# Kernel optimization log

Measured on AMD Instinct MI355X. Metric: run time of the kernel, lower is better.

The kernel has to match this reference:

```python
import jax, jax.numpy as jnp
import numpy as np

MARGIN_SCALE = 0.2
SPATIAL_ALPHA = 0.6
CHANNEL_ALPHA = 0.5
LANG_ALPHA = 0.4
EPS = 1e-06


def _xywh_to_xyxy(boxes):
    xc, yc, w, h = jnp.split(boxes, 4, axis=-1)
    return jnp.concatenate([xc - w / 2.0, yc - h / 2.0, xc + w / 2.0, yc + h / 2.0], axis=-1)


def _clamp_boxes(boxes):
    x1, y1, x2, y2 = [jnp.clip(b[..., 0], 0.0, 1.0) for b in jnp.split(boxes, 4, axis=-1)]
    x_low, x_high = jnp.minimum(x1, x2), jnp.maximum(x1, x2)
    y_low, y_high = jnp.minimum(y1, y2), jnp.maximum(y1, y2)
    w = jnp.maximum(x_high - x_low, EPS)
    h = jnp.maximum(y_high - y_low, EPS)
    cx = (x_high + x_low) * 0.5
    cy = (y_high + y_low) * 0.5
    return jnp.stack([
        jnp.clip(cx - w * 0.5, 0.0, 1.0),
        jnp.clip(cy - h * 0.5, 0.0, 1.0),
        jnp.clip(cx + w * 0.5, 0.0, 1.0),
        jnp.clip(cy + h * 0.5, 0.0, 1.0),
    ], axis=-1)


def _box_to_mask(boxes_xyxy, H, W, margin, dtype):
    # fully vectorized replacement of the per-sample Python loop
    ys = jnp.linspace(0.0, 1.0, H)  # [H]
    xs = jnp.linspace(0.0, 1.0, W)  # [W]
    x1, y1, x2, y2 = [boxes_xyxy[:, i] for i in range(4)]
    mx1 = jnp.clip(x1 - margin, 0.0, 1.0)[:, None, None]
    my1 = jnp.clip(y1 - margin, 0.0, 1.0)[:, None, None]
    mx2 = jnp.clip(x2 + margin, 0.0, 1.0)[:, None, None]
    my2 = jnp.clip(y2 + margin, 0.0, 1.0)[:, None, None]
    xg = xs[None, None, :]  # [1,1,W]
    yg = ys[None, :, None]  # [1,H,1]
    mask = (xg >= mx1) & (xg <= mx2) & (yg >= my1) & (yg <= my2)  # [B,H,W]
    return mask.astype(dtype)[:, None, :, :]  # [B,1,H,W]


def _conv2d(x, w, b, pad):
    out = jax.lax.conv_general_dilated(
        x, w, window_strides=(1, 1), padding=((pad, pad), (pad, pad)),
        dimension_numbers=('NCHW', 'OIHW', 'NCHW'))
    return out + b[None, :, None, None]


def setup_inputs() -> dict:
    key = jax.random.key(0)
    ks = jax.random.split(key, 9)
    B, C, H, W = 32, 256, 64, 64
    s = lambda fan_in: 1.0 / np.sqrt(fan_in)
    return {
        'feat': jax.random.normal(ks[0], (B, C, H, W), jnp.float32),
        'lang_vec': jax.random.normal(ks[1], (B, 256), jnp.float32),
        'pointer_xywh': jax.random.uniform(ks[2], (B, 4), jnp.float32),
        'conv1_w': jax.random.normal(ks[3], (16, 1, 3, 3), jnp.float32) * s(9),
        'conv1_b': jnp.zeros((16,), jnp.float32),
        'conv2_w': jax.random.normal(ks[4], (1, 16, 1, 1), jnp.float32) * s(16),
        'conv2_b': jnp.zeros((1,), jnp.float32),
        'cg_w1': jax.random.normal(ks[5], (256, 512), jnp.float32) * s(512),
        'cg_b1': jnp.zeros((256,), jnp.float32),
        'cg_w2': jax.random.normal(ks[6], (256, 256), jnp.float32) * s(256),
        'cg_b2': jnp.zeros((256,), jnp.float32),
        'lf_w1': jax.random.normal(ks[7], (256, 512), jnp.float32) * s(512),
        'lf_b1': jnp.zeros((256,), jnp.float32),
        'lf_w2': jax.random.normal(ks[8], (256, 256), jnp.float32) * s(256),
        'lf_b2': jnp.zeros((256,), jnp.float32),
    }


def reference(feat, lang_vec, pointer_xywh, conv1_w, conv1_b, conv2_w, conv2_b,
              cg_w1, cg_b1, cg_w2, cg_b2, lf_w1, lf_b1, lf_w2, lf_b2):
    B, C, H, W = feat.shape
    boxes_xyxy = _clamp_boxes(_xywh_to_xyxy(pointer_xywh))
    w = jnp.maximum(boxes_xyxy[:, 2] - boxes_xyxy[:, 0], 1e-4)
    h = jnp.maximum(boxes_xyxy[:, 3] - boxes_xyxy[:, 1], 1e-4)
    diag = jnp.sqrt(w * w + h * h)
    margin = jnp.clip(diag * MARGIN_SCALE, 0.02, 0.2)
    mask = _box_to_mask(boxes_xyxy, H, W, margin, feat.dtype)  # [B,1,H,W]

    # spatial gate: conv3x3 -> relu -> conv1x1 -> sigmoid
    hidden = jax.nn.relu(_conv2d(mask, conv1_w, conv1_b, pad=1))
    refined_mask = jax.nn.sigmoid(_conv2d(hidden, conv2_w, conv2_b, pad=0))  # [B,1,H,W]

    mask_area = jnp.maximum(refined_mask.sum(axis=(2, 3)), 1.0)  # [B,1]
    pointer_feat = (feat * refined_mask).sum(axis=(2, 3)) / mask_area  # [B,C]

    fusion = jnp.concatenate([pointer_feat, lang_vec], axis=1)  # [B, C+256]
    ch_gate = jax.nn.sigmoid(jax.nn.relu(fusion @ cg_w1.T + cg_b1) @ cg_w2.T + cg_b2)
    ch_gate = ch_gate.reshape(B, C, 1, 1)
    lang_delta = jnp.tanh(jax.nn.relu(fusion @ lf_w1.T + lf_b1) @ lf_w2.T + lf_b2)

    guided_feat = feat * (1.0 + SPATIAL_ALPHA * refined_mask) * (1.0 + CHANNEL_ALPHA * ch_gate)
    guided_lang = lang_vec + LANG_ALPHA * lang_delta
    return (guided_feat, guided_lang, boxes_xyxy, refined_mask, pointer_feat)
```

## Files before the change

### kernel.cpp

```cpp
#include <hip/hip_runtime.h>
#include <math.h>

#define B_  32
#define C_  256
#define H_  64
#define W_  64
#define HW  (H_*W_)
#define HW4 (HW/4)
#define RPB 4

typedef float f32x4 __attribute__((ext_vector_type(4)));

__device__ __forceinline__ float clamp01(float v) {
    return fminf(fmaxf(v, 0.0f), 1.0f);
}

__global__ __launch_bounds__(256) void kern_pf(
    const float* __restrict__ feat, const float* __restrict__ xywh,
    const float* __restrict__ conv1_w, const float* __restrict__ conv1_b,
    const float* __restrict__ conv2_w, const float* __restrict__ conv2_b,
    float* __restrict__ out_boxes, float* __restrict__ out_rm,
    float* __restrict__ out_pf)
{
    const int blk = blockIdx.x;
    const int b = blk >> 6;
    const int g = blk & 63;
    const int c0 = g * RPB;
    const int t = threadIdx.x;

    __shared__ float sw1[16 * 9];
    __shared__ float sb1[16];
    __shared__ float sw2[16];
    __shared__ float tbl[64];
    __shared__ int   xpat[64];
    __shared__ int   ypat[64];
    __shared__ f32x4 rm4_lds[HW4];
    __shared__ float sreda[4];
    __shared__ f32x4 sredv[4];

    float* rm_lds = (float*)rm4_lds;

    if (t < 144)                 sw1[t]       = conv1_w[t];
    else if (t < 160)            sb1[t - 144] = conv1_b[t - 144];
    else if (t < 176)            sw2[t - 160] = conv2_w[t - 160];
    const float b2v = conv2_b[0];

    const float xc = xywh[b * 4 + 0];
    const float yc = xywh[b * 4 + 1];
    const float bw = xywh[b * 4 + 2];
    const float bh = xywh[b * 4 + 3];

    float x1 = clamp01(xc - bw * 0.5f);
    float y1 = clamp01(yc - bh * 0.5f);
    float x2 = clamp01(xc + bw * 0.5f);
    float y2 = clamp01(yc + bh * 0.5f);
    float xl = fminf(x1, x2), xh = fmaxf(x1, x2);
    float yl = fminf(y1, y2), yh = fmaxf(y1, y2);
    float w_ = fmaxf(xh - xl, 1e-6f);
    float h_ = fmaxf(yh - yl, 1e-6f);
    float cx = (xh + xl) * 0.5f, cy = (yh + yl) * 0.5f;
    float bx1 = clamp01(cx - w_ * 0.5f);
    float by1 = clamp01(cy - h_ * 0.5f);
    float bx2 = clamp01(cx + w_ * 0.5f);
    float by2 = clamp01(cy + h_ * 0.5f);

    if (t == 0 && g == 0) {
        out_boxes[b * 4 + 0] = bx1;
        out_boxes[b * 4 + 1] = by1;
        out_boxes[b * 4 + 2] = bx2;
        out_boxes[b * 4 + 3] = by2;
    }

    float ww = fmaxf(bx2 - bx1, 1e-4f);
    float hh = fmaxf(by2 - by1, 1e-4f);
    float diag = sqrtf(ww * ww + hh * hh);
    float margin = fminf(fmaxf(diag * 0.2f, 0.02f), 0.2f);
    float mx1 = clamp01(bx1 - margin);
    float my1 = clamp01(by1 - margin);
    float mx2 = clamp01(bx2 + margin);
    float my2 = clamp01(by2 + margin);

    __syncthreads();

    if (t < 64) {
        const int x = t;
        int p = 0;
        #pragma unroll
        for (int k = 0; k < 3; ++k) {
            const int xx = x + k - 1;
            float gx = (float)((double)xx / 63.0);
            bool in = (xx >= 0) && (xx < W_) && (gx >= mx1) && (gx <= mx2);
            p |= (in ? 1 : 0) << k;
        }
        xpat[x] = p;
    } else if (t < 128) {
        const int y = t - 64;
        int p = 0;
        #pragma unroll
        for (int k = 0; k < 3; ++k) {
            const int yy = y + k - 1;
            float gy = (float)((double)yy / 63.0);
            bool in = (yy >= 0) && (yy < H_) && (gy >= my1) && (gy <= my2);
            p |= (in ? 1 : 0) << k;
        }
        ypat[y] = p;
    } else if (t < 192) {
        const int e = t - 128;
        const int xp = e & 7, yp = e >> 3;
        float mv[9];
        #pragma unroll
        for (int ky = 0; ky < 3; ++ky)
            #pragma unroll
            for (int kx = 0; kx < 3; ++kx)
                mv[ky * 3 + kx] = (((yp >> ky) & 1) && ((xp >> kx) & 1)) ? 1.0f : 0.0f;
        float z = b2v;
        #pragma unroll
        for (int oc = 0; oc < 16; ++oc) {
            float hsum = sb1[oc];
            #pragma unroll
            for (int k = 0; k < 9; ++k) hsum = fmaf(mv[k], sw1[oc * 9 + k], hsum);
            z = fmaf(fmaxf(hsum, 0.0f), sw2[oc], z);
        }
        tbl[e] = 1.0f / (1.0f + expf(-z));
    }
    __syncthreads();

    float asum = 0.0f;
    for (int p = t; p < HW; p += 256) {
        const int y = p >> 6;
        const int x = p & 63;
        float rm = tbl[ypat[y] * 8 + xpat[x]];
        rm_lds[p] = rm;
        asum += rm;
    }
    #pragma unroll
    for (int off = 32; off > 0; off >>= 1) asum += __shfl_down(asum, off, 64);
    const int lane = t & 63, wid = t >> 6;
    if (lane == 0) sreda[wid] = asum;
    __syncthreads();
    const float inv = 1.0f / fmaxf(sreda[0] + sreda[1] + sreda[2] + sreda[3], 1.0f);

    if (g == 0) {
        f32x4* orm = (f32x4*)(out_rm + (size_t)b * HW);
        for (int i = t; i < HW4; i += 256) orm[i] = rm4_lds[i];
    }

    const f32x4* fr = (const f32x4*)(feat + ((size_t)b * C_ + c0) * HW);
    float s0 = 0.f, s1 = 0.f, s2 = 0.f, s3 = 0.f;
    #pragma unroll 2
    for (int i = t; i < HW4; i += 256) {
        f32x4 r = rm4_lds[i];
        f32x4 f0 = fr[i];
        f32x4 f1 = fr[i + HW4];
        f32x4 f2 = fr[i + 2 * HW4];
        f32x4 f3 = fr[i + 3 * HW4];
        s0 = fmaf(f0.x, r.x, fmaf(f0.y, r.y, fmaf(f0.z, r.z, fmaf(f0.w, r.w, s0))));
        s1 = fmaf(f1.x, r.x, fmaf(f1.y, r.y, fmaf(f1.z, r.z, fmaf(f1.w, r.w, s1))));
        s2 = fmaf(f2.x, r.x, fmaf(f2.y, r.y, fmaf(f2.z, r.z, fmaf(f2.w, r.w, s2))));
        s3 = fmaf(f3.x, r.x, fmaf(f3.y, r.y, fmaf(f3.z, r.z, fmaf(f3.w, r.w, s3))));
    }

    #pragma unroll
    for (int off = 32; off > 0; off >>= 1) {
        s0 += __shfl_down(s0, off, 64);
        s1 += __shfl_down(s1, off, 64);
        s2 += __shfl_down(s2, off, 64);
        s3 += __shfl_down(s3, off, 64);
    }
    if (lane == 0) { f32x4 v; v.x = s0; v.y = s1; v.z = s2; v.w = s3; sredv[wid] = v; }
    __syncthreads();
    if (t == 0) {
        f32x4 t0 = sredv[0], t1 = sredv[1], t2 = sredv[2], t3 = sredv[3];
        out_pf[b * C_ + c0 + 0] = (t0.x + t1.x + t2.x + t3.x) * inv;
        out_pf[b * C_ + c0 + 1] = (t0.y + t1.y + t2.y + t3.y) * inv;
        out_pf[b * C_ + c0 + 2] = (t0.z + t1.z + t2.z + t3.z) * inv;
        out_pf[b * C_ + c0 + 3] = (t0.w + t1.w + t2.w + t3.w) * inv;
    }
}

__global__ __launch_bounds__(256) void kern_mlp(
    const float* __restrict__ pf, const float* __restrict__ lang,
    const float* __restrict__ cg_w1, const float* __restrict__ cg_b1,
    const float* __restrict__ cg_w2, const float* __restrict__ cg_b2,
    const float* __restrict__ lf_w1, const float* __restrict__ lf_b1,
    const float* __restrict__ lf_w2, const float* __restrict__ lf_b2,
    float* __restrict__ ws_cg, float* __restrict__ out_gl)
{
    const int b = blockIdx.x >> 1;
    const int which = blockIdx.x & 1;
    const int t = threadIdx.x;
    __shared__ float fus[512];
    __shared__ float hid[256];

    fus[t]       = pf[b * 256 + t];
    fus[256 + t] = lang[b * 256 + t];

    const float* w1 = which ? lf_w1 : cg_w1;
    const float* b1 = which ? lf_b1 : cg_b1;
    const float* w2 = which ? lf_w2 : cg_w2;
    const float* b2 = which ? lf_b2 : cg_b2;
    __syncthreads();

    const f32x4* wv = (const f32x4*)(w1 + (size_t)t * 512);
    const f32x4* fv = (const f32x4*)fus;
    float s = 0.0f;
    #pragma unroll 4
    for (int k = 0; k < 128; ++k) {
        f32x4 f = fv[k], w = wv[k];
        s = fmaf(f.x, w.x, fmaf(f.y, w.y, fmaf(f.z, w.z, fmaf(f.w, w.w, s))));
    }
    hid[t] = fmaxf(s + b1[t], 0.0f);
    __syncthreads();

    const f32x4* w2v = (const f32x4*)(w2 + (size_t)t * 256);
    const f32x4* hv = (const f32x4*)hid;
    float s2 = 0.0f;
    #pragma unroll 4
    for (int k = 0; k < 64; ++k) {
        f32x4 h = hv[k], w = w2v[k];
        s2 = fmaf(h.x, w.x, fmaf(h.y, w.y, fmaf(h.z, w.z, fmaf(h.w, w.w, s2))));
    }
    s2 += b2[t];
    if (which == 0) {
        ws_cg[b * 256 + t] = 1.0f + 0.5f / (1.0f + expf(-s2));
    } else {
        out_gl[b * 256 + t] = fus[256 + t] + 0.4f * tanhf(s2);
    }
}

__global__ __launch_bounds__(256) void kern_guided(
    const float* __restrict__ feat, const float* __restrict__ rm,
    const float* __restrict__ ws_cg, float* __restrict__ out_gf)
{
    const int blk = blockIdx.x;
    const int b = blk >> 6;
    const int c0 = (blk & 63) * RPB;
    const float g0 = ws_cg[b * C_ + c0 + 0];
    const float g1 = ws_cg[b * C_ + c0 + 1];
    const float g2 = ws_cg[b * C_ + c0 + 2];
    const float g3 = ws_cg[b * C_ + c0 + 3];

    const size_t row0 = ((size_t)b * C_ + c0) * HW;
    const f32x4* fr = (const f32x4*)(feat + row0);
    f32x4* orow = (f32x4*)(out_gf + row0);
    const f32x4* r4 = (const f32x4*)(rm + (size_t)b * HW);

    #pragma unroll 2
    for (int i = threadIdx.x; i < HW4; i += 256) {
        f32x4 r = r4[i];
        f32x4 m;
        m.x = 1.0f + 0.6f * r.x;
        m.y = 1.0f + 0.6f * r.y;
        m.z = 1.0f + 0.6f * r.z;
        m.w = 1.0f + 0.6f * r.w;
        f32x4 f0 = fr[i];
        f32x4 f1 = fr[i + HW4];
        f32x4 f2 = fr[i + 2 * HW4];
        f32x4 f3 = fr[i + 3 * HW4];
        f32x4 o0, o1, o2, o3;
        o0.x = f0.x * m.x * g0; o0.y = f0.y * m.y * g0;
        o0.z = f0.z * m.z * g0; o0.w = f0.w * m.w * g0;
        o1.x = f1.x * m.x * g1; o1.y = f1.y * m.y * g1;
        o1.z = f1.z * m.z * g1; o1.w = f1.w * m.w * g1;
        o2.x = f2.x * m.x * g2; o2.y = f2.y * m.y * g2;
        o2.z = f2.z * m.z * g2; o2.w = f2.w * m.w * g2;
        o3.x = f3.x * m.x * g3; o3.y = f3.y * m.y * g3;
        o3.z = f3.z * m.z * g3; o3.w = f3.w * m.w * g3;
        __builtin_nontemporal_store(o0, &orow[i]);
        __builtin_nontemporal_store(o1, &orow[i + HW4]);
        __builtin_nontemporal_store(o2, &orow[i + 2 * HW4]);
        __builtin_nontemporal_store(o3, &orow[i + 3 * HW4]);
    }
}

extern "C" void kernel_launch(void* const* d_in, const int* in_sizes, int n_in,
                              void* d_out, int out_size, void* d_ws, size_t ws_size,
                              hipStream_t stream) {
    const float* feat     = (const float*)d_in[0];
    const float* lang     = (const float*)d_in[1];
    const float* xywh     = (const float*)d_in[2];
    const float* conv1_w  = (const float*)d_in[3];
    const float* conv1_b  = (const float*)d_in[4];
    const float* conv2_w  = (const float*)d_in[5];
    const float* conv2_b  = (const float*)d_in[6];
    const float* cg_w1    = (const float*)d_in[7];
    const float* cg_b1    = (const float*)d_in[8];
    const float* cg_w2    = (const float*)d_in[9];
    const float* cg_b2    = (const float*)d_in[10];
    const float* lf_w1    = (const float*)d_in[11];
    const float* lf_b1    = (const float*)d_in[12];
    const float* lf_w2    = (const float*)d_in[13];
    const float* lf_b2    = (const float*)d_in[14];

    float* out = (float*)d_out;
    const size_t N_GF = (size_t)B_ * C_ * HW;
    float* out_gf    = out;
    float* out_gl    = out_gf + N_GF;
    float* out_boxes = out_gl + (size_t)B_ * C_;
    float* out_rm    = out_boxes + B_ * 4;
    float* out_pf    = out_rm + (size_t)B_ * HW;

    float* wsf   = (float*)d_ws;
    float* ws_cg = wsf;

    (void)ws_size; (void)in_sizes; (void)n_in; (void)out_size;

    kern_pf<<<B_ * C_ / RPB, 256, 0, stream>>>(feat, xywh,
                                               conv1_w, conv1_b, conv2_w, conv2_b,
                                               out_boxes, out_rm, out_pf);
    kern_mlp<<<B_ * 2, 256, 0, stream>>>(out_pf, lang,
                                         cg_w1, cg_b1, cg_w2, cg_b2,
                                         lf_w1, lf_b1, lf_w2, lf_b2,
                                         ws_cg, out_gl);
    kern_guided<<<B_ * C_ / RPB, 256, 0, stream>>>(feat, out_rm, ws_cg, out_gf);
}
```

Before: 95.09 us.

## Fuse pooling, MLP and guided scaling into one cooperative kernel with grid syncs

Replaces the three-launch pipeline with a single cooperative kernel. Each block handles 8 channels of one sample: it computes the refined mask and pooled features, grid-syncs, runs the MLP in the first 64 blocks, grid-syncs again, then writes guided features with nontemporal stores. The goal is to cut launch overhead, keep the mask in LDS, and re-read each feat slice soon after its first read so it is more likely to hit cache. The cost is two grid-wide barriers and idle blocks during the MLP phase; if occupancy is too low for a cooperative launch, it falls back to the old three-kernel path.

```diff
diff --git a/kernel.cpp b/kernel.cpp
--- a/kernel.cpp
+++ b/kernel.cpp
@@ -1,4 +1,5 @@
 #include <hip/hip_runtime.h>
+#include <hip/hip_cooperative_groups.h>
 #include <math.h>
 
 #define B_  32
@@ -7,12 +8,272 @@
 #define W_  64
 #define HW  (H_*W_)
 #define HW4 (HW/4)
+#define MRPB 8
 #define RPB 4
+
+namespace cg = cooperative_groups;
 
 typedef float f32x4 __attribute__((ext_vector_type(4)));
 
 __device__ __forceinline__ float clamp01(float v) {
     return fminf(fmaxf(v, 0.0f), 1.0f);
+}
+
+struct BoxParams {
+    float bx1, by1, bx2, by2, mx1, my1, mx2, my2;
+};
+
+__device__ __forceinline__ BoxParams box_math(const float* __restrict__ xywh, int b) {
+    const float xc = xywh[b * 4 + 0];
+    const float yc = xywh[b * 4 + 1];
+    const float bw = xywh[b * 4 + 2];
+    const float bh = xywh[b * 4 + 3];
+
+    float x1 = clamp01(xc - bw * 0.5f);
+    float y1 = clamp01(yc - bh * 0.5f);
+    float x2 = clamp01(xc + bw * 0.5f);
+    float y2 = clamp01(yc + bh * 0.5f);
+    float xl = fminf(x1, x2), xh = fmaxf(x1, x2);
+    float yl = fminf(y1, y2), yh = fmaxf(y1, y2);
+    float w_ = fmaxf(xh - xl, 1e-6f);
+    float h_ = fmaxf(yh - yl, 1e-6f);
+    float cx = (xh + xl) * 0.5f, cy = (yh + yl) * 0.5f;
+    BoxParams p;
+    p.bx1 = clamp01(cx - w_ * 0.5f);
+    p.by1 = clamp01(cy - h_ * 0.5f);
+    p.bx2 = clamp01(cx + w_ * 0.5f);
+    p.by2 = clamp01(cy + h_ * 0.5f);
+    float ww = fmaxf(p.bx2 - p.bx1, 1e-4f);
+    float hh = fmaxf(p.by2 - p.by1, 1e-4f);
+    float diag = sqrtf(ww * ww + hh * hh);
+    float margin = fminf(fmaxf(diag * 0.2f, 0.02f), 0.2f);
+    p.mx1 = clamp01(p.bx1 - margin);
+    p.my1 = clamp01(p.by1 - margin);
+    p.mx2 = clamp01(p.bx2 + margin);
+    p.my2 = clamp01(p.by2 + margin);
+    return p;
+}
+
+__device__ __forceinline__ void build_tables(
+    int t, const BoxParams& p, float b2v,
+    const float* sw1, const float* sb1, const float* sw2,
+    int* xpat, int* ypat, float* tbl)
+{
+    if (t < 64) {
+        const int x = t;
+        int pp = 0;
+        #pragma unroll
+        for (int k = 0; k < 3; ++k) {
+            const int xx = x + k - 1;
+            float gx = (float)((double)xx / 63.0);
+            bool in = (xx >= 0) && (xx < W_) && (gx >= p.mx1) && (gx <= p.mx2);
+            pp |= (in ? 1 : 0) << k;
+        }
+        xpat[x] = pp;
+    } else if (t < 128) {
+        const int y = t - 64;
+        int pp = 0;
+        #pragma unroll
+        for (int k = 0; k < 3; ++k) {
+            const int yy = y + k - 1;
+            float gy = (float)((double)yy / 63.0);
+            bool in = (yy >= 0) && (yy < H_) && (gy >= p.my1) && (gy <= p.my2);
+            pp |= (in ? 1 : 0) << k;
+        }
+        ypat[y] = pp;
+    } else if (t < 192) {
+        const int e = t - 128;
+        const int xp = e & 7, yp = e >> 3;
+        float mv[9];
+        #pragma unroll
+        for (int ky = 0; ky < 3; ++ky)
+            #pragma unroll
+            for (int kx = 0; kx < 3; ++kx)
+                mv[ky * 3 + kx] = (((yp >> ky) & 1) && ((xp >> kx) & 1)) ? 1.0f : 0.0f;
+        float z = b2v;
+        #pragma unroll
+        for (int oc = 0; oc < 16; ++oc) {
+            float hsum = sb1[oc];
+            #pragma unroll
+            for (int k = 0; k < 9; ++k) hsum = fmaf(mv[k], sw1[oc * 9 + k], hsum);
+            z = fmaf(fmaxf(hsum, 0.0f), sw2[oc], z);
+        }
+        tbl[e] = 1.0f / (1.0f + expf(-z));
+    }
+}
+
+__global__ __launch_bounds__(256, 4) void kern_mega(
+    const float* __restrict__ feat, const float* __restrict__ lang,
+    const float* __restrict__ xywh,
+    const float* __restrict__ conv1_w, const float* __restrict__ conv1_b,
+    const float* __restrict__ conv2_w, const float* __restrict__ conv2_b,
+    const float* __restrict__ cg_w1, const float* __restrict__ cg_b1,
+    const float* __restrict__ cg_w2, const float* __restrict__ cg_b2,
+    const float* __restrict__ lf_w1, const float* __restrict__ lf_b1,
+    const float* __restrict__ lf_w2, const float* __restrict__ lf_b2,
+    float* __restrict__ out_gf, float* __restrict__ out_gl,
+    float* __restrict__ out_boxes, float* __restrict__ out_rm,
+    float* __restrict__ out_pf, float* __restrict__ ws_cg)
+{
+    cg::grid_group grid = cg::this_grid();
+
+    const int blk = blockIdx.x;
+    const int b = blk >> 5;
+    const int g = blk & 31;
+    const int c0 = g * MRPB;
+    const int t = threadIdx.x;
+
+    __shared__ f32x4 rm4_lds[HW4];
+    __shared__ __align__(16) char scratch[3072];
+
+    float* sw1   = (float*)(scratch);
+    float* sb1   = (float*)(scratch + 576);
+    float* sw2   = (float*)(scratch + 640);
+    float* tbl   = (float*)(scratch + 704);
+    int*   xpat  = (int*)  (scratch + 960);
+    int*   ypat  = (int*)  (scratch + 1216);
+    float* sreda = (float*)(scratch + 1472);
+    float* sredp = (float*)(scratch + 1536);
+    float* fus   = (float*)(scratch);
+    float* hid   = (float*)(scratch + 2048);
+
+    float* rm_lds = (float*)rm4_lds;
+
+    if (t < 144)                 sw1[t]       = conv1_w[t];
+    else if (t < 160)            sb1[t - 144] = conv1_b[t - 144];
+    else if (t < 176)            sw2[t - 160] = conv2_w[t - 160];
+    const float b2v = conv2_b[0];
+
+    const BoxParams bp = box_math(xywh, b);
+    if (t == 0 && g == 0) {
+        out_boxes[b * 4 + 0] = bp.bx1;
+        out_boxes[b * 4 + 1] = bp.by1;
+        out_boxes[b * 4 + 2] = bp.bx2;
+        out_boxes[b * 4 + 3] = bp.by2;
+    }
+    __syncthreads();
+
+    build_tables(t, bp, b2v, sw1, sb1, sw2, xpat, ypat, tbl);
+    __syncthreads();
+
+    float asum = 0.0f;
+    for (int p = t; p < HW; p += 256) {
+        const int y = p >> 6;
+        const int x = p & 63;
+        float rm = tbl[ypat[y] * 8 + xpat[x]];
+        rm_lds[p] = rm;
+        asum += rm;
+    }
+    #pragma unroll
+    for (int off = 32; off > 0; off >>= 1) asum += __shfl_down(asum, off, 64);
+    const int lane = t & 63, wid = t >> 6;
+    if (lane == 0) sreda[wid] = asum;
+    __syncthreads();
+    const float inv = 1.0f / fmaxf(sreda[0] + sreda[1] + sreda[2] + sreda[3], 1.0f);
+
+    if (g == 0) {
+        f32x4* orm = (f32x4*)(out_rm + (size_t)b * HW);
+        for (int i = t; i < HW4; i += 256) orm[i] = rm4_lds[i];
+    }
+
+    const size_t row0 = ((size_t)b * C_ + c0) * HW;
+    const f32x4* fr = (const f32x4*)(feat + row0);
+    {
+        float s[MRPB];
+        #pragma unroll
+        for (int j = 0; j < MRPB; ++j) s[j] = 0.0f;
+        for (int i = t; i < HW4; i += 256) {
+            f32x4 r = rm4_lds[i];
+            #pragma unroll
+            for (int j = 0; j < MRPB; ++j) {
+                f32x4 f = fr[i + j * HW4];
+                s[j] = fmaf(f.x, r.x, fmaf(f.y, r.y, fmaf(f.z, r.z, fmaf(f.w, r.w, s[j]))));
+            }
+        }
+        #pragma unroll
+        for (int j = 0; j < MRPB; ++j) {
+            #pragma unroll
+            for (int off = 32; off > 0; off >>= 1) s[j] += __shfl_down(s[j], off, 64);
+        }
+        if (lane == 0) {
+            #pragma unroll
+            for (int j = 0; j < MRPB; ++j) sredp[wid * MRPB + j] = s[j];
+        }
+        __syncthreads();
+        if (t < MRPB) {
+            float tot = sredp[0 * MRPB + t] + sredp[1 * MRPB + t] +
+                        sredp[2 * MRPB + t] + sredp[3 * MRPB + t];
+            out_pf[b * C_ + c0 + t] = tot * inv;
+        }
+    }
+
+    grid.sync();
+
+    if (blk < 64) {
+        const int bb = blk >> 1;
+        const int which = blk & 1;
+
+        fus[t]       = out_pf[bb * 256 + t];
+        fus[256 + t] = lang[bb * 256 + t];
+
+        const float* w1 = which ? lf_w1 : cg_w1;
+        const float* b1 = which ? lf_b1 : cg_b1;
+        const float* w2 = which ? lf_w2 : cg_w2;
+        const float* b2 = which ? lf_b2 : cg_b2;
+        __syncthreads();
+
+        const f32x4* wv = (const f32x4*)(w1 + (size_t)t * 512);
+        const f32x4* fv = (const f32x4*)fus;
+        float s = 0.0f;
+        #pragma unroll 4
+        for (int k = 0; k < 128; ++k) {
+            f32x4 f = fv[k], w = wv[k];
+            s = fmaf(f.x, w.x, fmaf(f.y, w.y, fmaf(f.z, w.z, fmaf(f.w, w.w, s))));
+        }
+        hid[t] = fmaxf(s + b1[t], 0.0f);
+        __syncthreads();
+
+        const f32x4* w2v = (const f32x4*)(w2 + (size_t)t * 256);
+        const f32x4* hv = (const f32x4*)hid;
+        float s2 = 0.0f;
+        #pragma unroll 4
+        for (int k = 0; k < 64; ++k) {
+            f32x4 h = hv[k], w = w2v[k];
+            s2 = fmaf(h.x, w.x, fmaf(h.y, w.y, fmaf(h.z, w.z, fmaf(h.w, w.w, s2))));
+        }
+        s2 += b2[t];
+        if (which == 0) {
+            ws_cg[bb * 256 + t] = 1.0f + 0.5f / (1.0f + expf(-s2));
+        } else {
+            out_gl[bb * 256 + t] = fus[256 + t] + 0.4f * tanhf(s2);
+        }
+    }
+
+    grid.sync();
+
+    float gr[MRPB];
+    #pragma unroll
+    for (int j = 0; j < MRPB; ++j) gr[j] = ws_cg[b * C_ + c0 + j];
+
+    f32x4* orow = (f32x4*)(out_gf + row0);
+    for (int i = t; i < HW4; i += 256) {
+        f32x4 r = rm4_lds[i];
+        f32x4 m;
+        m.x = 1.0f + 0.6f * r.x;
+        m.y = 1.0f + 0.6f * r.y;
+        m.z = 1.0f + 0.6f * r.z;
+        m.w = 1.0f + 0.6f * r.w;
+        #pragma unroll
+        for (int j = 0; j < MRPB; ++j) {
+            f32x4 f = fr[i + j * HW4];
+            f32x4 o;
+            o.x = f.x * m.x * gr[j];
+            o.y = f.y * m.y * gr[j];
+            o.z = f.z * m.z * gr[j];
+            o.w = f.w * m.w * gr[j];
+            __builtin_nontemporal_store(o, &orow[i + j * HW4]);
+        }
+    }
 }
 
 __global__ __launch_bounds__(256) void kern_pf(
@@ -45,84 +306,16 @@
     else if (t < 176)            sw2[t - 160] = conv2_w[t - 160];
     const float b2v = conv2_b[0];
 
-    const float xc = xywh[b * 4 + 0];
-    const float yc = xywh[b * 4 + 1];
-    const float bw = xywh[b * 4 + 2];
-    const float bh = xywh[b * 4 + 3];
-
-    float x1 = clamp01(xc - bw * 0.5f);
-    float y1 = clamp01(yc - bh * 0.5f);
-    float x2 = clamp01(xc + bw * 0.5f);
-    float y2 = clamp01(yc + bh * 0.5f);
-    float xl = fminf(x1, x2), xh = fmaxf(x1, x2);
-    float yl = fminf(y1, y2), yh = fmaxf(y1, y2);
-    float w_ = fmaxf(xh - xl, 1e-6f);
-    float h_ = fmaxf(yh - yl, 1e-6f);
-    float cx = (xh + xl) * 0.5f, cy = (yh + yl) * 0.5f;
-    float bx1 = clamp01(cx - w_ * 0.5f);
-    float by1 = clamp01(cy - h_ * 0.5f);
-    float bx2 = clamp01(cx + w_ * 0.5f);
-    float by2 = clamp01(cy + h_ * 0.5f);
-
+    const BoxParams bp = box_math(xywh, b);
     if (t == 0 && g == 0) {
-        out_boxes[b * 4 + 0] = bx1;
-        out_boxes[b * 4 + 1] = by1;
-        out_boxes[b * 4 + 2] = bx2;
-        out_boxes[b * 4 + 3] = by2;
-    }
-
-    float ww = fmaxf(bx2 - bx1, 1e-4f);
-    float hh = fmaxf(by2 - by1, 1e-4f);
-    float diag = sqrtf(ww * ww + hh * hh);
-    float margin = fminf(fmaxf(diag * 0.2f, 0.02f), 0.2f);
-    float mx1 = clamp01(bx1 - margin);
-    float my1 = clamp01(by1 - margin);
-    float mx2 = clamp01(bx2 + margin);
-    float my2 = clamp01(by2 + margin);
-
-    __syncthreads();
-
-    if (t < 64) {
-        const int x = t;
-        int p = 0;
-        #pragma unroll
-        for (int k = 0; k < 3; ++k) {
-            const int xx = x + k - 1;
-            float gx = (float)((double)xx / 63.0);
-            bool in = (xx >= 0) && (xx < W_) && (gx >= mx1) && (gx <= mx2);
-            p |= (in ? 1 : 0) << k;
-        }
-        xpat[x] = p;
-    } else if (t < 128) {
-        const int y = t - 64;
-        int p = 0;
-        #pragma unroll
-        for (int k = 0; k < 3; ++k) {
-            const int yy = y + k - 1;
-            float gy = (float)((double)yy / 63.0);
-            bool in = (yy >= 0) && (yy < H_) && (gy >= my1) && (gy <= my2);
-            p |= (in ? 1 : 0) << k;
-        }
-        ypat[y] = p;
-    } else if (t < 192) {
-        const int e = t - 128;
-        const int xp = e & 7, yp = e >> 3;
-        float mv[9];
-        #pragma unroll
-        for (int ky = 0; ky < 3; ++ky)
-            #pragma unroll
-            for (int kx = 0; kx < 3; ++kx)
-                mv[ky * 3 + kx] = (((yp >> ky) & 1) && ((xp >> kx) & 1)) ? 1.0f : 0.0f;
-        float z = b2v;
-        #pragma unroll
-        for (int oc = 0; oc < 16; ++oc) {
-            float hsum = sb1[oc];
-            #pragma unroll
-            for (int k = 0; k < 9; ++k) hsum = fmaf(mv[k], sw1[oc * 9 + k], hsum);
-            z = fmaf(fmaxf(hsum, 0.0f), sw2[oc], z);
-        }
-        tbl[e] = 1.0f / (1.0f + expf(-z));
-    }
+        out_boxes[b * 4 + 0] = bp.bx1;
+        out_boxes[b * 4 + 1] = bp.by1;
+        out_boxes[b * 4 + 2] = bp.bx2;
+        out_boxes[b * 4 + 3] = bp.by2;
+    }
+    __syncthreads();
+
+    build_tables(t, bp, b2v, sw1, sb1, sw2, xpat, ypat, tbl);
     __syncthreads();
 
     float asum = 0.0f;
@@ -159,7 +352,6 @@
         s2 = fmaf(f2.x, r.x, fmaf(f2.y, r.y, fmaf(f2.z, r.z, fmaf(f2.w, r.w, s2))));
         s3 = fmaf(f3.x, r.x, fmaf(f3.y, r.y, fmaf(f3.z, r.z, fmaf(f3.w, r.w, s3))));
     }
-
     #pragma unroll
     for (int off = 32; off > 0; off >>= 1) {
         s0 += __shfl_down(s0, off, 64);
@@ -300,17 +492,35 @@
     float* out_rm    = out_boxes + B_ * 4;
     float* out_pf    = out_rm + (size_t)B_ * HW;
 
-    float* wsf   = (float*)d_ws;
-    float* ws_cg = wsf;
+    float* ws_cg = (float*)d_ws;
 
     (void)ws_size; (void)in_sizes; (void)n_in; (void)out_size;
 
-    kern_pf<<<B_ * C_ / RPB, 256, 0, stream>>>(feat, xywh,
-                                               conv1_w, conv1_b, conv2_w, conv2_b,
-                                               out_boxes, out_rm, out_pf);
-    kern_mlp<<<B_ * 2, 256, 0, stream>>>(out_pf, lang,
-                                         cg_w1, cg_b1, cg_w2, cg_b2,
-                                         lf_w1, lf_b1, lf_w2, lf_b2,
-                                         ws_cg, out_gl);
-    kern_guided<<<B_ * C_ / RPB, 256, 0, stream>>>(feat, out_rm, ws_cg, out_gf);
-}
+    const int MEGA_GRID = B_ * C_ / MRPB;
+    int nb = 0;
+    hipError_t oe = hipOccupancyMaxActiveBlocksPerMultiprocessor(&nb, kern_mega, 256, 0);
+    const bool coop_ok = (oe == hipSuccess) && (nb * 256 >= MEGA_GRID);
+
+    if (coop_ok) {
+        void* args[] = {
+            (void*)&feat, (void*)&lang, (void*)&xywh,
+            (void*)&conv1_w, (void*)&conv1_b, (void*)&conv2_w, (void*)&conv2_b,
+            (void*)&cg_w1, (void*)&cg_b1, (void*)&cg_w2, (void*)&cg_b2,
+            (void*)&lf_w1, (void*)&lf_b1, (void*)&lf_w2, (void*)&lf_b2,
+            (void*)&out_gf, (void*)&out_gl, (void*)&out_boxes, (void*)&out_rm,
+            (void*)&out_pf, (void*)&ws_cg
+        };
+        hipLaunchCooperativeKernel((const void*)kern_mega,
+                                   dim3(MEGA_GRID), dim3(256),
+                                   args, 0, stream);
+    } else {
+        kern_pf<<<B_ * C_ / RPB, 256, 0, stream>>>(feat, xywh,
+                                                   conv1_w, conv1_b, conv2_w, conv2_b,
+                                                   out_boxes, out_rm, out_pf);
+        kern_mlp<<<B_ * 2, 256, 0, stream>>>(out_pf, lang,
+                                             cg_w1, cg_b1, cg_w2, cg_b2,
+                                             lf_w1, lf_b1, lf_w2, lf_b2,
+                                             ws_cg, out_gl);
+        kern_guided<<<B_ * C_ / RPB, 256, 0, stream>>>(feat, out_rm, ws_cg, out_gf);
+    }
+}
```

Result: no change. 94.29 us (-0.8%).
